# Performance work log

Hardware: AMD Instinct MI355X
Metric: run time of the kernel (lower is better)

The kernel has to match this reference:

```python
import jax, jax.numpy as jnp
import numpy as np

EPS = 1e-8

def setup_inputs() -> dict:
    key = jax.random.key(0)
    ks = jax.random.split(key, 7)
    B, S, H, NH, V = 4, 2048, 1024, 8, 2048
    sc = 1.0 / np.sqrt(H)
    return {
        "hidden": jax.random.normal(ks[0], (B, S, H), jnp.float32),
        "prior_w": jax.random.normal(ks[1], (H, NH), jnp.float32) * sc,
        "prior_b": jnp.zeros((NH,), jnp.float32),
        "latent_w": jax.random.normal(ks[2], (H, NH * H), jnp.float32) * sc,
        "latent_b": jnp.zeros((NH * H,), jnp.float32),
        "output_w": jax.random.normal(ks[3], (H, V), jnp.float32) * sc,
        "output_b": jnp.zeros((V,), jnp.float32),
    }

def reference(hidden, prior_w, prior_b, latent_w, latent_b, output_w, output_b):
    B, S, H = hidden.shape
    NH = prior_w.shape[1]
    # prior: sigmoid then renormalize over heads
    prior = jax.nn.sigmoid(hidden @ prior_w + prior_b)              # [B,S,NH]
    prior = prior / (prior.sum(-1, keepdims=True) + EPS)
    # latent: linear -> [B,S,NH,H] -> tanh
    latent = jnp.tanh((hidden @ latent_w + latent_b).reshape(B, S, NH, H))
    # per-head softmax over vocab, weighted sum over heads
    logits = jnp.einsum('bsnh,hv->bsnv', latent, output_w) + output_b
    probs = jax.nn.softmax(logits, axis=-1)                          # [B,S,NH,V]
    return jnp.einsum('bsn,bsnv->bsv', prior, probs)
```

## Files before the change

### kernel.cpp

```cpp
#include <hip/hip_runtime.h>
#include <hip/hip_bf16.h>
#include <stdint.h>

typedef _Float16 f16;
typedef _Float16 f16x8 __attribute__((ext_vector_type(8)));
typedef _Float16 f16x4 __attribute__((ext_vector_type(4)));
typedef float f32x4 __attribute__((ext_vector_type(4)));

#define T_TOK 8192
#define H_DIM 1024
#define NHEAD 8
#define V_DIM 2048

__device__ __forceinline__ void gload16(const void* g, void* l) {
  __builtin_amdgcn_global_load_lds(
      (const __attribute__((address_space(1))) void*)(uintptr_t)g,
      (__attribute__((address_space(3))) void*)(unsigned)(uintptr_t)l,
      16, 0, 0);
}

__device__ __forceinline__ float fast_tanh(float x) {
  float xc = fminf(fmaxf(x, -12.f), 12.f);
  float e = __expf(2.f * xc);
  return (e - 1.f) / (e + 1.f);
}

__device__ __forceinline__ void stage_half(const f16* __restrict__ gRowBase,
                                           char* ldsHalf, int tid, int sl8,
                                           int Kd) {
  const int srow = tid >> 3;
  char* wuni = ldsHalf + ((tid >> 6) << 10);
  gload16(gRowBase + (size_t)srow * Kd + sl8, wuni);
  gload16(gRowBase + (size_t)(srow + 64) * Kd + sl8, wuni + 8192);
}

template <int TANH>
__global__ __launch_bounds__(512, 2) void k_gemm(const f16* __restrict__ A,
                                                 const f16* __restrict__ Bt,
                                                 const float* __restrict__ bias,
                                                 f16* __restrict__ C,
                                                 int M, int N, int K) {
  __shared__ __align__(16) f16 sA[2][16384];
  __shared__ __align__(16) f16 sB[2][16384];
  const int tid = threadIdx.x;
  const int lane = tid & 63;
  const int wid = tid >> 6;
  const int wr = wid >> 2, wc = wid & 3;
  const int gx = gridDim.x;
  const int id = blockIdx.y * gx + blockIdx.x;
  const int cpx = (gx * gridDim.y) >> 3;
  const int sw = (id & 7) * cpx + (id >> 3);
  const int m0 = (sw / gx) * 256, n0 = (sw % gx) * 256;
  const int NT = K >> 6;
  const int sl8 = ((tid & 7) ^ ((tid >> 3) & 7)) << 3;
  const int lo15 = lane & 15;
  const int offk0 = lo15 * 128 + (((lane >> 4)) ^ (lane & 7)) * 16;
  const int offk1 = lo15 * 128 + ((4 + (lane >> 4)) ^ (lane & 7)) * 16;

  const f16* Ag = A + (size_t)m0 * K;
  const f16* Bg = Bt + (size_t)n0 * K;
  char* sAb = (char*)&sA[0][0];
  char* sBb = (char*)&sB[0][0];

  stage_half(Ag, sAb, tid, sl8, K);
  stage_half(Ag + (size_t)128 * K, sAb + 16384, tid, sl8, K);
  stage_half(Bg, sBb, tid, sl8, K);
  stage_half(Bg + (size_t)128 * K, sBb + 16384, tid, sl8, K);
  stage_half(Bg + 64, sBb + 32768, tid, sl8, K);
  stage_half(Bg + (size_t)128 * K + 64, sBb + 32768 + 16384, tid, sl8, K);
  asm volatile("s_waitcnt vmcnt(4)" ::: "memory");
  __builtin_amdgcn_s_barrier();
  __builtin_amdgcn_sched_barrier(0);

  f32x4 acc[8][4] = {};
  f16x8 af0[4], af1[4], bf[4][2];

#define LDA_SET(dst, base, q)                                                  \
  {                                                                            \
    dst[0] = *(const f16x8*)((base) + wr * 16384 + (2 * (q) + 0) * 2048 + offk0); \
    dst[1] = *(const f16x8*)((base) + wr * 16384 + (2 * (q) + 0) * 2048 + offk1); \
    dst[2] = *(const f16x8*)((base) + wr * 16384 + (2 * (q) + 1) * 2048 + offk0); \
    dst[3] = *(const f16x8*)((base) + wr * 16384 + (2 * (q) + 1) * 2048 + offk1); \
  }
#define LDB(base)                                                              \
  {                                                                            \
    _Pragma("unroll") for (int ni = 0; ni < 4; ++ni) {                         \
      bf[ni][0] = *(const f16x8*)((base) + wc * 8192 + ni * 2048 + offk0);     \
      bf[ni][1] = *(const f16x8*)((base) + wc * 8192 + ni * 2048 + offk1);     \
    }                                                                          \
  }
#define MFMA16(q, S)                                                           \
  {                                                                            \
    __builtin_amdgcn_s_setprio(1);                                             \
    _Pragma("unroll") for (int ni = 0; ni < 4; ++ni) {                         \
      acc[2 * (q) + 0][ni] = __builtin_amdgcn_mfma_f32_16x16x32_f16(           \
          S[0], bf[ni][0], acc[2 * (q) + 0][ni], 0, 0, 0);                     \
      acc[2 * (q) + 0][ni] = __builtin_amdgcn_mfma_f32_16x16x32_f16(           \
          S[1], bf[ni][1], acc[2 * (q) + 0][ni], 0, 0, 0);                     \
      acc[2 * (q) + 1][ni] = __builtin_amdgcn_mfma_f32_16x16x32_f16(           \
          S[2], bf[ni][0], acc[2 * (q) + 1][ni], 0, 0, 0);                     \
      acc[2 * (q) + 1][ni] = __builtin_amdgcn_mfma_f32_16x16x32_f16(           \
          S[3], bf[ni][1], acc[2 * (q) + 1][ni], 0, 0, 0);                     \
    }                                                                          \
    __builtin_amdgcn_s_setprio(0);                                             \
  }

  LDA_SET(af0, sAb, 0);

#define HALF(tt, bc)                                                           \
  {                                                                            \
    const char* cA = sAb + (bc)*32768;                                         \
    const char* cB = sBb + (bc)*32768;                                         \
    char* nA = sAb + ((bc) ^ 1) * 32768;                                       \
    char* nB = sBb + (bc)*32768;                                               \
    const int ktA = ((tt) + 1) << 6, ktB = ((tt) + 2) << 6;                    \
    const bool doA = (tt) + 1 < NT, doB = (tt) + 2 < NT;                       \
                                    \
    if (doA) stage_half(Ag + ktA, nA, tid, sl8, K);                            \
    LDB(cB);                                                                   \
    LDA_SET(af1, cA, 1);                                                       \
    __builtin_amdgcn_sched_barrier(0);                                         \
    MFMA16(0, af0);                                                            \
    __builtin_amdgcn_s_barrier();                                              \
                                                                      \
    if (doA) stage_half(Ag + (size_t)128 * K + ktA, nA + 16384, tid, sl8, K);  \
    LDA_SET(af0, cA, 2);                                                       \
    __builtin_amdgcn_sched_barrier(0);                                         \
    MFMA16(1, af1);                                                            \
    __builtin_amdgcn_s_barrier();                                              \
                                                                      \
    if (doB) stage_half(Bg + ktB, nB, tid, sl8, K);                            \
    LDA_SET(af1, cA, 3);                                                       \
    __builtin_amdgcn_sched_barrier(0);                                         \
    MFMA16(2, af0);                                                            \
    __builtin_amdgcn_s_barrier();                                              \
                  \
    if (doB) stage_half(Bg + (size_t)128 * K + ktB, nB + 16384, tid, sl8, K);  \
    if (doB) {                                                                 \
      asm volatile("s_waitcnt vmcnt(4)" ::: "memory");                         \
    } else {                                                                   \
      asm volatile("s_waitcnt vmcnt(0)" ::: "memory");                         \
    }                                                                          \
    __builtin_amdgcn_s_barrier();                                              \
    __builtin_amdgcn_sched_barrier(0);                                         \
    if (doA) LDA_SET(af0, sAb + ((bc) ^ 1) * 32768, 0);                        \
    __builtin_amdgcn_sched_barrier(0);                                         \
    MFMA16(3, af1);                                                            \
  }

#pragma unroll 1
  for (int T = 0; T < NT; T += 2) {
    HALF(T, 0);
    HALF(T + 1, 1);
  }
#undef HALF
#undef LDA_SET
#undef LDB
#undef MFMA16

  const int crow = m0 + wr * 128 + ((lane >> 4) << 2);
  const int ccol0 = n0 + wc * 64 + lo15;
  float bv[4];
#pragma unroll
  for (int ni = 0; ni < 4; ++ni) bv[ni] = bias[ccol0 + ni * 16];
#pragma unroll
  for (int mi = 0; mi < 8; ++mi) {
#pragma unroll
    for (int r = 0; r < 4; ++r) {
      f16* Crow = C + (size_t)(crow + mi * 16 + r) * N;
#pragma unroll
      for (int ni = 0; ni < 4; ++ni) {
        float v = acc[mi][ni][r] + bv[ni];
        if (TANH) v = fast_tanh(v);
        Crow[ccol0 + ni * 16] = (f16)v;
      }
    }
  }
}

__global__ __launch_bounds__(256) void k_convert(const float* __restrict__ in,
                                                 f16* __restrict__ out, int n4) {
  int i = blockIdx.x * blockDim.x + threadIdx.x;
  if (i >= n4) return;
  const float4 v = ((const float4*)in)[i];
  f16x4 o;
  o[0] = (f16)v.x; o[1] = (f16)v.y; o[2] = (f16)v.z; o[3] = (f16)v.w;
  ((f16x4*)out)[i] = o;
}

__global__ void k_transpose(const float* __restrict__ in, f16* __restrict__ out,
                            int R, int C) {
  __shared__ f16 tile[32][33];
  int c0 = blockIdx.x * 32, r0 = blockIdx.y * 32;
  for (int j = threadIdx.y; j < 32; j += 8)
    tile[j][threadIdx.x] = (f16)in[(size_t)(r0 + j) * C + (c0 + threadIdx.x)];
  __syncthreads();
  for (int j = threadIdx.y; j < 32; j += 8)
    out[(size_t)(c0 + j) * R + (r0 + threadIdx.x)] = tile[threadIdx.x][j];
}

__global__ __launch_bounds__(256) void k_prior(const float* __restrict__ hidden,
                                               const float* __restrict__ pw,
                                               const float* __restrict__ pb,
                                               float* __restrict__ prior) {
  const int wid = threadIdx.x >> 6, lane = threadIdx.x & 63;
  const int t = blockIdx.x * 4 + wid;
  float acc[NHEAD] = {0.f, 0.f, 0.f, 0.f, 0.f, 0.f, 0.f, 0.f};
  const float* hrow = hidden + (size_t)t * H_DIM;
  for (int k = lane; k < H_DIM; k += 64) {
    float x = hrow[k];
    const float* wr = pw + k * NHEAD;
#pragma unroll
    for (int h = 0; h < NHEAD; ++h) acc[h] += x * wr[h];
  }
#pragma unroll
  for (int h = 0; h < NHEAD; ++h) {
#pragma unroll
    for (int off = 32; off >= 1; off >>= 1) acc[h] += __shfl_xor(acc[h], off);
  }
  if (lane == 0) {
    float p[NHEAD], s = 0.f;
#pragma unroll
    for (int h = 0; h < NHEAD; ++h) {
      p[h] = 1.f / (1.f + __expf(-(acc[h] + pb[h])));
      s += p[h];
    }
    float inv = 1.f / (s + 1e-8f);
#pragma unroll
    for (int h = 0; h < NHEAD; ++h) prior[t * NHEAD + h] = p[h] * inv;
  }
}

__global__ __launch_bounds__(256) void k_softmax(const f16* __restrict__ logits,
                                                 const float* __restrict__ prior,
                                                 float* __restrict__ out) {
  __shared__ float red[4];
  const int t = blockIdx.x;
  const int tid = threadIdx.x, lane = tid & 63, wid = tid >> 6;
  float oa[8] = {0.f, 0.f, 0.f, 0.f, 0.f, 0.f, 0.f, 0.f};
  const int v0 = tid * 8;
#pragma unroll 1
  for (int h = 0; h < NHEAD; ++h) {
    f16x8 x = *(const f16x8*)(logits + ((size_t)t * NHEAD + h) * V_DIM + v0);
    float xv[8], mx = -1e30f;
#pragma unroll
    for (int j = 0; j < 8; j++) { xv[j] = (float)x[j]; mx = fmaxf(mx, xv[j]); }
#pragma unroll
    for (int off = 32; off >= 1; off >>= 1) mx = fmaxf(mx, __shfl_xor(mx, off));
    if (lane == 0) red[wid] = mx;
    __syncthreads();
    mx = fmaxf(fmaxf(red[0], red[1]), fmaxf(red[2], red[3]));
    __syncthreads();
    float e[8], s = 0.f;
#pragma unroll
    for (int j = 0; j < 8; j++) { e[j] = __expf(xv[j] - mx); s += e[j]; }
#pragma unroll
    for (int off = 32; off >= 1; off >>= 1) s += __shfl_xor(s, off);
    if (lane == 0) red[wid] = s;
    __syncthreads();
    s = red[0] + red[1] + red[2] + red[3];
    __syncthreads();
    const float coef = prior[t * NHEAD + h] / s;
#pragma unroll
    for (int j = 0; j < 8; j++) oa[j] += coef * e[j];
  }
  float4* op = (float4*)(out + (size_t)t * V_DIM + v0);
  op[0] = make_float4(oa[0], oa[1], oa[2], oa[3]);
  op[1] = make_float4(oa[4], oa[5], oa[6], oa[7]);
}

extern "C" void kernel_launch(void* const* d_in, const int* in_sizes, int n_in,
                              void* d_out, int out_size, void* d_ws, size_t ws_size,
                              hipStream_t stream) {
  const float* hidden   = (const float*)d_in[0];
  const float* prior_w  = (const float*)d_in[1];
  const float* prior_b  = (const float*)d_in[2];
  const float* latent_w = (const float*)d_in[3];
  const float* latent_b = (const float*)d_in[4];
  const float* output_w = (const float*)d_in[5];
  const float* output_b = (const float*)d_in[6];
  float* out = (float*)d_out;

  char* ws = (char*)d_ws;
  size_t off = 0;
  auto alloc = [&](size_t bytes) -> void* {
    void* p = ws + off;
    off += (bytes + 255) & ~(size_t)255;
    return p;
  };
  f16* hidden_h = (f16*)alloc((size_t)T_TOK * H_DIM * 2);
  f16* lw_t     = (f16*)alloc((size_t)NHEAD * H_DIM * H_DIM * 2);
  f16* ow_t     = (f16*)alloc((size_t)V_DIM * H_DIM * 2);
  float* prior  = (float*)alloc((size_t)T_TOK * NHEAD * 4);

  int tc = 2048;
  while (tc > 256) {
    size_t need = off + (size_t)tc * NHEAD * H_DIM * 2 + 256 +
                  (size_t)tc * NHEAD * V_DIM * 2 + 256;
    if (need <= ws_size) break;
    tc >>= 1;
  }
  f16* latent_h = (f16*)alloc((size_t)tc * NHEAD * H_DIM * 2);
  f16* logits_h = (f16*)alloc((size_t)tc * NHEAD * V_DIM * 2);

  k_convert<<<(T_TOK * H_DIM / 4 + 255) / 256, 256, 0, stream>>>(
      hidden, hidden_h, T_TOK * H_DIM / 4);
  k_transpose<<<dim3(NHEAD * H_DIM / 32, H_DIM / 32), dim3(32, 8), 0, stream>>>(
      latent_w, lw_t, H_DIM, NHEAD * H_DIM);
  k_transpose<<<dim3(V_DIM / 32, H_DIM / 32), dim3(32, 8), 0, stream>>>(
      output_w, ow_t, H_DIM, V_DIM);
  k_prior<<<T_TOK / 4, 256, 0, stream>>>(hidden, prior_w, prior_b, prior);

  const int nchunk = T_TOK / tc;
  for (int c = 0; c < nchunk; ++c) {
    const f16* Ah = hidden_h + (size_t)c * tc * H_DIM;
    k_gemm<1><<<dim3(NHEAD * H_DIM / 256, tc / 256), 512, 0, stream>>>(
        Ah, lw_t, latent_b, latent_h, tc, NHEAD * H_DIM, H_DIM);
    k_gemm<0><<<dim3(V_DIM / 256, tc * NHEAD / 256), 512, 0, stream>>>(
        latent_h, ow_t, output_b, logits_h, tc * NHEAD, V_DIM, H_DIM);
    k_softmax<<<tc, 256, 0, stream>>>(logits_h, prior + (size_t)c * tc * NHEAD,
                                      out + (size_t)c * tc * V_DIM);
  }
}
```

Before: 583.0 us.

## Switch GEMM to 32x32x16 MFMA tiles and enlarge token chunk size

Replaces the 16x16x32 MFMA instruction with 32x32x16 MFMA in the main GEMM, and rewrites the LDS fragment addressing, accumulator layout and epilogue store mapping to match. The larger MFMA tile cuts the number of LDS fragment loads per FLOP and the instruction issue count. The token chunk size now starts at the full token count, so fewer chunked launches are needed when the workspace is large enough. This uses more workspace memory, and the epilogue writes 32-wide column strips with a different store pattern.

```diff
diff --git a/kernel.cpp b/kernel.cpp
--- a/kernel.cpp
+++ b/kernel.cpp
@@ -6,6 +6,7 @@
 typedef _Float16 f16x8 __attribute__((ext_vector_type(8)));
 typedef _Float16 f16x4 __attribute__((ext_vector_type(4)));
 typedef float f32x4 __attribute__((ext_vector_type(4)));
+typedef float f32x16 __attribute__((ext_vector_type(16)));
 
 #define T_TOK 8192
 #define H_DIM 1024
@@ -53,9 +54,9 @@
   const int m0 = (sw / gx) * 256, n0 = (sw % gx) * 256;
   const int NT = K >> 6;
   const int sl8 = ((tid & 7) ^ ((tid >> 3) & 7)) << 3;
-  const int lo15 = lane & 15;
-  const int offk0 = lo15 * 128 + (((lane >> 4)) ^ (lane & 7)) * 16;
-  const int offk1 = lo15 * 128 + ((4 + (lane >> 4)) ^ (lane & 7)) * 16;
+  const int rr31 = lane & 31;
+  const int hi = lane >> 5;
+  const int l7 = lane & 7;
 
   const f16* Ag = A + (size_t)m0 * K;
   const f16* Bg = Bt + (size_t)n0 * K;
@@ -72,35 +73,33 @@
   __builtin_amdgcn_s_barrier();
   __builtin_amdgcn_sched_barrier(0);
 
-  f32x4 acc[8][4] = {};
-  f16x8 af0[4], af1[4], bf[4][2];
+  f32x16 acc[4][2] = {};
+  f16x8 af0[4], af1[4], bf[2][4];
 
 #define LDA_SET(dst, base, q)                                                  \
   {                                                                            \
-    dst[0] = *(const f16x8*)((base) + wr * 16384 + (2 * (q) + 0) * 2048 + offk0); \
-    dst[1] = *(const f16x8*)((base) + wr * 16384 + (2 * (q) + 0) * 2048 + offk1); \
-    dst[2] = *(const f16x8*)((base) + wr * 16384 + (2 * (q) + 1) * 2048 + offk0); \
-    dst[3] = *(const f16x8*)((base) + wr * 16384 + (2 * (q) + 1) * 2048 + offk1); \
+    _Pragma("unroll") for (int mi = 0; mi < 4; ++mi) {                         \
+      dst[mi] = *(const f16x8*)((base) + wr * 16384 + mi * 4096 + rr31 * 128 + \
+                                (((2 * (q) + hi) ^ l7) << 4));                 \
+    }                                                                          \
   }
 #define LDB(base)                                                              \
   {                                                                            \
-    _Pragma("unroll") for (int ni = 0; ni < 4; ++ni) {                         \
-      bf[ni][0] = *(const f16x8*)((base) + wc * 8192 + ni * 2048 + offk0);     \
-      bf[ni][1] = *(const f16x8*)((base) + wc * 8192 + ni * 2048 + offk1);     \
+    _Pragma("unroll") for (int n = 0; n < 2; ++n) {                            \
+      _Pragma("unroll") for (int ks = 0; ks < 4; ++ks) {                       \
+        bf[n][ks] = *(const f16x8*)((base) + wc * 8192 + n * 4096 +            \
+                                    rr31 * 128 + (((2 * ks + hi) ^ l7) << 4)); \
+      }                                                                        \
     }                                                                          \
   }
-#define MFMA16(q, S)                                                           \
+#define MFMA8(ks, S)                                                           \
   {                                                                            \
     __builtin_amdgcn_s_setprio(1);                                             \
-    _Pragma("unroll") for (int ni = 0; ni < 4; ++ni) {                         \
-      acc[2 * (q) + 0][ni] = __builtin_amdgcn_mfma_f32_16x16x32_f16(           \
-          S[0], bf[ni][0], acc[2 * (q) + 0][ni], 0, 0, 0);                     \
-      acc[2 * (q) + 0][ni] = __builtin_amdgcn_mfma_f32_16x16x32_f16(           \
-          S[1], bf[ni][1], acc[2 * (q) + 0][ni], 0, 0, 0);                     \
-      acc[2 * (q) + 1][ni] = __builtin_amdgcn_mfma_f32_16x16x32_f16(           \
-          S[2], bf[ni][0], acc[2 * (q) + 1][ni], 0, 0, 0);                     \
-      acc[2 * (q) + 1][ni] = __builtin_amdgcn_mfma_f32_16x16x32_f16(           \
-          S[3], bf[ni][1], acc[2 * (q) + 1][ni], 0, 0, 0);                     \
+    _Pragma("unroll") for (int mi = 0; mi < 4; ++mi) {                         \
+      _Pragma("unroll") for (int n = 0; n < 2; ++n) {                          \
+        acc[mi][n] = __builtin_amdgcn_mfma_f32_32x32x16_f16(                   \
+            S[mi], bf[n][ks], acc[mi][n], 0, 0, 0);                            \
+      }                                                                        \
     }                                                                          \
     __builtin_amdgcn_s_setprio(0);                                             \
   }
@@ -115,24 +114,24 @@
     char* nB = sBb + (bc)*32768;                                               \
     const int ktA = ((tt) + 1) << 6, ktB = ((tt) + 2) << 6;                    \
     const bool doA = (tt) + 1 < NT, doB = (tt) + 2 < NT;                       \
-                                    \
+                                                                      \
     if (doA) stage_half(Ag + ktA, nA, tid, sl8, K);                            \
     LDB(cB);                                                                   \
     LDA_SET(af1, cA, 1);                                                       \
     __builtin_amdgcn_sched_barrier(0);                                         \
-    MFMA16(0, af0);                                                            \
+    MFMA8(0, af0);                                                             \
     __builtin_amdgcn_s_barrier();                                              \
                                                                       \
     if (doA) stage_half(Ag + (size_t)128 * K + ktA, nA + 16384, tid, sl8, K);  \
     LDA_SET(af0, cA, 2);                                                       \
     __builtin_amdgcn_sched_barrier(0);                                         \
-    MFMA16(1, af1);                                                            \
+    MFMA8(1, af1);                                                             \
     __builtin_amdgcn_s_barrier();                                              \
                                                                       \
     if (doB) stage_half(Bg + ktB, nB, tid, sl8, K);                            \
     LDA_SET(af1, cA, 3);                                                       \
     __builtin_amdgcn_sched_barrier(0);                                         \
-    MFMA16(2, af0);                                                            \
+    MFMA8(2, af0);                                                             \
     __builtin_amdgcn_s_barrier();                                              \
                   \
     if (doB) stage_half(Bg + (size_t)128 * K + ktB, nB + 16384, tid, sl8, K);  \
@@ -145,7 +144,7 @@
     __builtin_amdgcn_sched_barrier(0);                                         \
     if (doA) LDA_SET(af0, sAb + ((bc) ^ 1) * 32768, 0);                        \
     __builtin_amdgcn_sched_barrier(0);                                         \
-    MFMA16(3, af1);                                                            \
+    MFMA8(3, af1);                                                             \
   }
 
 #pragma unroll 1
@@ -156,23 +155,26 @@
 #undef HALF
 #undef LDA_SET
 #undef LDB
-#undef MFMA16
-
-  const int crow = m0 + wr * 128 + ((lane >> 4) << 2);
-  const int ccol0 = n0 + wc * 64 + lo15;
-  float bv[4];
-#pragma unroll
-  for (int ni = 0; ni < 4; ++ni) bv[ni] = bias[ccol0 + ni * 16];
-#pragma unroll
-  for (int mi = 0; mi < 8; ++mi) {
-#pragma unroll
-    for (int r = 0; r < 4; ++r) {
-      f16* Crow = C + (size_t)(crow + mi * 16 + r) * N;
-#pragma unroll
-      for (int ni = 0; ni < 4; ++ni) {
-        float v = acc[mi][ni][r] + bv[ni];
-        if (TANH) v = fast_tanh(v);
-        Crow[ccol0 + ni * 16] = (f16)v;
+#undef MFMA8
+
+  const int ccol0 = n0 + wc * 64 + rr31;
+  float bv[2];
+#pragma unroll
+  for (int n = 0; n < 2; ++n) bv[n] = bias[ccol0 + n * 32];
+#pragma unroll
+  for (int mi = 0; mi < 4; ++mi) {
+#pragma unroll
+    for (int rq = 0; rq < 4; ++rq) {
+#pragma unroll
+      for (int r2 = 0; r2 < 4; ++r2) {
+        const int row = m0 + wr * 128 + mi * 32 + r2 + 8 * rq + 4 * hi;
+        f16* Crow = C + (size_t)row * N;
+#pragma unroll
+        for (int n = 0; n < 2; ++n) {
+          float v = acc[mi][n][rq * 4 + r2] + bv[n];
+          if (TANH) v = fast_tanh(v);
+          Crow[ccol0 + n * 32] = (f16)v;
+        }
       }
     }
   }
@@ -293,7 +295,7 @@
   f16* ow_t     = (f16*)alloc((size_t)V_DIM * H_DIM * 2);
   float* prior  = (float*)alloc((size_t)T_TOK * NHEAD * 4);
 
-  int tc = 2048;
+  int tc = T_TOK;
   while (tc > 256) {
     size_t need = off + (size_t)tc * NHEAD * H_DIM * 2 + 256 +
                   (size_t)tc * NHEAD * V_DIM * 2 + 256;
```

After: 600.2 us. 1.03x slower.
